# Kernel tuning notes

Hardware: AMD Instinct MI355X
Metric: run time of the kernel (lower is better)

Reference implementation:

```python
import jax, jax.numpy as jnp
import numpy as np

B, C, N = 8, 3, 4096
NSAMPLE = 10
MLP = (64, 64)
# checkerboard re-gather pattern from the original module
INDS = np.array([0, 1, 2, 3, 2, 3, 4, 5, 4, 5, 6, 7, 6, 7, 8, 9])


def setup_inputs() -> dict:
    key = jax.random.key(0)
    k1, k2, k3 = jax.random.split(key, 3)
    pos = jax.random.normal(k1, (B, C, N), jnp.float32)
    w1 = jax.random.normal(k2, (MLP[0], 4 * C, 2, 2), jnp.float32) * 0.1  # Conv2d(12, mlp0, k=2)
    b1 = jnp.zeros((MLP[0],), jnp.float32)
    w2 = jax.random.normal(k3, (MLP[1], MLP[0]), jnp.float32) * 0.1       # Conv2d(mlp0, mlp1, k=1)
    b2 = jnp.zeros((MLP[1],), jnp.float32)
    return {"pos": pos, "w1": w1, "b1": b1, "w2": w2, "b2": b2}


def _squeeze_2x2_alt(x):
    # x: [B, N, c, 4, 4] -> [B, N, 4c, 2, 2] with channel order [a, d, b, c]
    a = x[..., 0::2, 0::2]  # (0,0) of each 2x2 block
    d = x[..., 1::2, 1::2]  # (1,1)
    b = x[..., 0::2, 1::2]  # (0,1)
    c = x[..., 1::2, 0::2]  # (1,0)
    return jnp.concatenate([a, d, b, c], axis=-3)


def reference(pos, w1, b1, w2, b2):
    Bn, Cn, Nn = pos.shape
    pos_t = pos.transpose(0, 2, 1)  # [B, N, C]
    # pairwise squared distances [B, N, N]
    sq = jnp.sum(pos_t * pos_t, axis=-1)
    d2 = sq[:, :, None] - 2.0 * jnp.einsum('bnc,bmc->bnm', pos_t, pos_t) + sq[:, None, :]
    _, idx = jax.lax.top_k(-d2, NSAMPLE)  # [B, N, K] nearest neighbors (self first)
    # grouping_operation: grouped[b,c,n,k] = pos[b,c,idx[b,n,k]]
    grouped = jax.vmap(lambda p, i: p[:, i])(pos, idx)  # [B, C, N, K]
    pg = grouped[..., INDS]                              # [B, C, N, 16]
    pg = pg.transpose(0, 2, 1, 3).reshape(Bn, Nn, Cn, 4, 4)  # [B, N, 3, 4, 4]
    sqz = _squeeze_2x2_alt(pg)                           # [B, N, 12, 2, 2]
    # Conv2d(12->mlp0, k=2, stride=1) over 2x2 spatial == full contraction
    h = jnp.einsum('bnchw,ochw->bno', sqz, w1) + b1      # [B, N, mlp0]
    out = jnp.einsum('bno,po->bnp', h, w2) + b2          # [B, N, mlp1]
    return out.transpose(0, 2, 1)                        # [B, mlp1, N]
```

## Files before the change

### kernel.cpp

```cpp
#include <hip/hip_runtime.h>
#include <math.h>

#define NPTS 4096
#define NSMP 10

typedef float f32x2 __attribute__((ext_vector_type(2)));

__global__ __launch_bounds__(256) void prep_kernel(
    const float* __restrict__ w1, const float* __restrict__ b1,
    const float* __restrict__ w2, const float* __restrict__ b2,
    float* __restrict__ wn, float* __restrict__ bb) {
  __shared__ float w1l[64 * 48];
  __shared__ float w2t[64 * 64];
  __shared__ float b1l[64];
  __shared__ float part[4][30][64];
  __shared__ float bpart[4][64];
  const int t = threadIdx.x, p = t & 63, grp = t >> 6, o0 = grp * 16;
  for (int idx = t; idx < 64 * 48; idx += 256) w1l[idx] = w1[idx];
  for (int idx = t; idx < 64 * 64; idx += 256) w2t[(idx & 63) * 64 + (idx >> 6)] = w2[idx];
  if (t < 64) b1l[t] = b1[t];
  __syncthreads();

  const int sg[16] = {0,2,4,6, 3,5,7,9, 1,3,5,7, 2,4,6,8};
  float w2r[16];
  #pragma unroll
  for (int oo = 0; oo < 16; ++oo) w2r[oo] = w2t[(o0 + oo) * 64 + p];
  float wloc[30];
  #pragma unroll
  for (int i = 0; i < 30; ++i) wloc[i] = 0.0f;
  #pragma unroll
  for (int g = 0; g < 4; ++g)
    #pragma unroll
    for (int i = 0; i < 2; ++i)
      #pragma unroll
      for (int j = 0; j < 2; ++j) {
        const int s = sg[g * 4 + i * 2 + j];
        #pragma unroll
        for (int c = 0; c < 3; ++c) {
          const int k = (c + 3 * g) * 4 + i * 2 + j;
          float wk = 0.0f;
          #pragma unroll
          for (int oo = 0; oo < 16; ++oo)
            wk = fmaf(w2r[oo], w1l[(o0 + oo) * 48 + k], wk);
          wloc[s * 3 + c] += wk;
        }
      }
  #pragma unroll
  for (int i = 0; i < 30; ++i) part[grp][i][p] = wloc[i];
  float sb = 0.0f;
  #pragma unroll
  for (int oo = 0; oo < 16; ++oo) sb = fmaf(w2r[oo], b1l[o0 + oo], sb);
  bpart[grp][p] = sb;
  __syncthreads();
  const float* p0 = &part[0][0][0];
  for (int idx = t; idx < 30 * 64; idx += 256)
    wn[idx] = p0[idx] + p0[1920 + idx] + p0[3840 + idx] + p0[5760 + idx];
  if (t < 64) bb[t] = b2[t] + bpart[0][t] + bpart[1][t] + bpart[2][t] + bpart[3][t];
}

__global__ __launch_bounds__(1024, 8) void topk_kernel(const float* __restrict__ pos,
                                                       const float* __restrict__ wng,
                                                       const float* __restrict__ bbg,
                                                       float* __restrict__ out) {
  __shared__ float pts3[NPTS * 3];
  __shared__ float trans[16 * 260];
  __shared__ float wl[30 * 64];
  __shared__ float bl[64];
  __shared__ int   nbrL[16][4][NSMP];
  __shared__ int   cnt[16][4];

  const int b = blockIdx.y, tid = threadIdx.x, lane = tid & 63, wv = tid >> 6;
  const float* pb = pos + (size_t)b * 3 * NPTS;
  for (int i = tid; i < NPTS; i += 1024) {
    pts3[3 * i + 0] = pb[i];
    pts3[3 * i + 1] = pb[i + NPTS];
    pts3[3 * i + 2] = pb[i + 2 * NPTS];
  }
  for (int i = tid; i < 30 * 64; i += 1024) wl[i] = wng[i];
  if (tid < 64) bl[tid] = bbg[tid];
  __syncthreads();

  const int nb = blockIdx.x * 64;
  const int n0 = nb + wv * 4;
  float* transF = &trans[wv * 260];
  int*   bufiW  = (int*)transF;

  f32x2 qx2[2], qy2[2], qz2[2], dmin[2];
  #pragma unroll
  for (int pp = 0; pp < 2; ++pp) {
    int na = n0 + 2 * pp;
    qx2[pp].x = -2.0f * pts3[3 * na + 0]; qx2[pp].y = -2.0f * pts3[3 * na + 3];
    qy2[pp].x = -2.0f * pts3[3 * na + 1]; qy2[pp].y = -2.0f * pts3[3 * na + 4];
    qz2[pp].x = -2.0f * pts3[3 * na + 2]; qz2[pp].y = -2.0f * pts3[3 * na + 5];
    dmin[pp].x = INFINITY; dmin[pp].y = INFINITY;
  }

  #pragma unroll 2
  for (int k = 0; k < 64; ++k) {
    int m = k * 64 + lane;
    float x = pts3[3 * m], y = pts3[3 * m + 1], z = pts3[3 * m + 2];
    float sq = fmaf(z, z, fmaf(y, y, x * x));
    f32x2 sq2; sq2.x = sq; sq2.y = sq;
    #pragma unroll
    for (int pp = 0; pp < 2; ++pp) {
      f32x2 key = qx2[pp] * x + sq2;
      key = qy2[pp] * y + key;
      key = qz2[pp] * z + key;
      dmin[pp] = __builtin_elementwise_min(dmin[pp], key);
    }
  }

  unsigned um[4];
  #pragma unroll
  for (int r = 0; r < 4; ++r) {
    float dm = (r & 1) ? dmin[r >> 1].y : dmin[r >> 1].x;
    unsigned ub = __float_as_uint(dm);
    um[r] = (ub & 0x80000000u) ? ~ub : (ub | 0x80000000u);
  }
  unsigned pfx0 = 0u, pfx1 = 0u, pfx2 = 0u, pfx3 = 0u;
  #pragma unroll 1
  for (int bno = 31; bno >= 8; --bno) {
    const unsigned bit = 1u << bno, ones = bit - 1u;
    if (__popcll(__ballot(um[0] <= (pfx0 | ones))) < NSMP) pfx0 |= bit;
    if (__popcll(__ballot(um[1] <= (pfx1 | ones))) < NSMP) pfx1 |= bit;
    if (__popcll(__ballot(um[2] <= (pfx2 | ones))) < NSMP) pfx2 |= bit;
    if (__popcll(__ballot(um[3] <= (pfx3 | ones))) < NSMP) pfx3 |= bit;
  }
  float tx[4];
  #pragma unroll
  for (int r = 0; r < 4; ++r) {
    unsigned T = ((r == 0) ? pfx0 : (r == 1) ? pfx1 : (r == 2) ? pfx2 : pfx3) | 0xFFu;
    unsigned tb = (T & 0x80000000u) ? (T ^ 0x80000000u) : ~T;
    float tf = __uint_as_float(tb);
    tx[r] = __fadd_rn(__fadd_rn(tf, 2e-4f), __fmul_rn(fabsf(tf), 1e-5f));
  }

  if (lane < 4) cnt[wv][lane] = 0;

  #pragma unroll 2
  for (int k = 0; k < 64; ++k) {
    int m = k * 64 + lane;
    float x = pts3[3 * m], y = pts3[3 * m + 1], z = pts3[3 * m + 2];
    float sq = fmaf(z, z, fmaf(y, y, x * x));
    f32x2 sq2; sq2.x = sq; sq2.y = sq;
    #pragma unroll
    for (int pp = 0; pp < 2; ++pp) {
      f32x2 key = qx2[pp] * x + sq2;
      key = qy2[pp] * y + key;
      key = qz2[pp] * z + key;
      if (key.x <= tx[2 * pp]) {
        int ps = atomicAdd(&cnt[wv][2 * pp], 1);
        if (ps < 64) bufiW[(2 * pp) * 64 + ps] = m;
      }
      if (key.y <= tx[2 * pp + 1]) {
        int ps = atomicAdd(&cnt[wv][2 * pp + 1], 1);
        if (ps < 64) bufiW[(2 * pp + 1) * 64 + ps] = m;
      }
    }
  }

  int c[4], si[4], rank[4];
  double dd[4];
  int cmax = 0;
  #pragma unroll
  for (int r = 0; r < 4; ++r) {
    c[r] = __builtin_amdgcn_readfirstlane(cnt[wv][r]);
    if (c[r] > 64) c[r] = 64;
    cmax = (c[r] > cmax) ? c[r] : cmax;
    rank[r] = 0;
  }
  #pragma unroll
  for (int r = 0; r < 4; ++r) {
    int nq = n0 + r;
    float qxf = pts3[3 * nq], qyf = pts3[3 * nq + 1], qzf = pts3[3 * nq + 2];
    if (lane < c[r]) {
      si[r] = bufiW[r * 64 + lane];
      float px = pts3[3 * si[r]], py = pts3[3 * si[r] + 1], pz = pts3[3 * si[r] + 2];
      double dqx = (double)qxf, dqy = (double)qyf, dqz = (double)qzf;
      double dpx = (double)px, dpy = (double)py, dpz = (double)pz;
      double dot = dqx * dpx + dqy * dpy + dqz * dpz;
      double sqn = dqx * dqx + dqy * dqy + dqz * dqz;
      double sqm = dpx * dpx + dpy * dpy + dpz * dpz;
      dd[r] = (sqn - 2.0 * dot) + sqm;
    } else { dd[r] = (double)INFINITY; si[r] = 0x7FFFFFFF; }
  }
  #pragma unroll 1
  for (int j = 0; j < cmax; ++j) {
    #pragma unroll
    for (int r = 0; r < 4; ++r) {
      int jlo = __builtin_amdgcn_readlane(__double2loint(dd[r]), j);
      int jhi = __builtin_amdgcn_readlane(__double2hiint(dd[r]), j);
      int ji  = __builtin_amdgcn_readlane(si[r], j);
      double jd = __hiloint2double(jhi, jlo);
      if (jd < dd[r] || (jd == dd[r] && ji < si[r])) ++rank[r];
    }
  }
  #pragma unroll
  for (int r = 0; r < 4; ++r)
    if (lane < c[r] && rank[r] < NSMP)
      nbrL[wv][r][rank[r]] = si[r];

  #pragma unroll 1
  for (int r = 0; r < 4; ++r) {
    float a = bl[lane];
    #pragma unroll
    for (int s = 0; s < NSMP; ++s) {
      int id = nbrL[wv][r][s];
      float px = pts3[3 * id], py = pts3[3 * id + 1], pz = pts3[3 * id + 2];
      a = fmaf(wl[(s * 3 + 0) * 64 + lane], px, a);
      a = fmaf(wl[(s * 3 + 1) * 64 + lane], py, a);
      a = fmaf(wl[(s * 3 + 2) * 64 + lane], pz, a);
    }
    transF[r * 65 + lane] = a;
  }
  __syncthreads();

  {
    int p = tid >> 4, t16 = tid & 15;
    float4 v;
    v.x = trans[t16 * 260 + 0 * 65 + p];
    v.y = trans[t16 * 260 + 1 * 65 + p];
    v.z = trans[t16 * 260 + 2 * 65 + p];
    v.w = trans[t16 * 260 + 3 * 65 + p];
    *(float4*)(out + ((size_t)b * 64 + p) * NPTS + nb + 4 * t16) = v;
  }
}

extern "C" void kernel_launch(void* const* d_in, const int* in_sizes, int n_in,
                              void* d_out, int out_size, void* d_ws, size_t ws_size,
                              hipStream_t stream) {
  (void)in_sizes; (void)n_in; (void)out_size; (void)ws_size;
  const float* pos = (const float*)d_in[0];
  const float* w1  = (const float*)d_in[1];
  const float* b1  = (const float*)d_in[2];
  const float* w2  = (const float*)d_in[3];
  const float* b2  = (const float*)d_in[4];
  float* out = (float*)d_out;

  float* wn = (float*)d_ws;
  float* bb = (float*)((char*)d_ws + 30 * 64 * 4);

  prep_kernel<<<dim3(1), dim3(256), 0, stream>>>(w1, b1, w2, b2, wn, bb);
  topk_kernel<<<dim3(64, 8), dim3(1024), 0, stream>>>(pos, wn, bb, out);
}
```

Before: 131.5 us.

## Compute kNN distance keys with fp16 split-precision MFMA instead of scalar FMAs

Both distance passes (the min-per-lane threshold pass and the candidate-collection pass) now run as 32x32x16 f16 MFMA products. Each point is stored as hi/lo fp16 pairs of x, y, z and the squared norm, so the matrix product approximates -2q·p+|p|^2. Work is reassigned so each wave covers a slice of 512 candidates for 32 queries. Per-lane minima go to shared memory to form the radix-select input, and atomics collect candidates per query row. To absorb the reduced precision, the threshold slack now scales with the query's magnitude, and exact fp64 re-ranking plus the final MLP gather read coordinates from global memory. The changes add barriers and cut occupancy hints from 8 to 4, and a looser threshold risks more candidates or overflow past 64.

```diff
diff --git a/kernel.cpp b/kernel.cpp
--- a/kernel.cpp
+++ b/kernel.cpp
@@ -5,6 +5,8 @@
 #define NSMP 10
 
 typedef float f32x2 __attribute__((ext_vector_type(2)));
+typedef _Float16 half8 __attribute__((ext_vector_type(8)));
+typedef float f32x16 __attribute__((ext_vector_type(16)));
 
 __global__ __launch_bounds__(256) void prep_kernel(
     const float* __restrict__ w1, const float* __restrict__ b1,
@@ -58,62 +60,90 @@
   if (t < 64) bb[t] = b2[t] + bpart[0][t] + bpart[1][t] + bpart[2][t] + bpart[3][t];
 }
 
-__global__ __launch_bounds__(1024, 8) void topk_kernel(const float* __restrict__ pos,
+__global__ __launch_bounds__(1024, 4) void topk_kernel(const float* __restrict__ pos,
                                                        const float* __restrict__ wng,
                                                        const float* __restrict__ bbg,
                                                        float* __restrict__ out) {
-  __shared__ float pts3[NPTS * 3];
-  __shared__ float trans[16 * 260];
+  __shared__ half8 pts8[NPTS];
+  __shared__ float X[16 * 260];
+  __shared__ half8 a8[128];
   __shared__ float wl[30 * 64];
   __shared__ float bl[64];
-  __shared__ int   nbrL[16][4][NSMP];
-  __shared__ int   cnt[16][4];
+  __shared__ float taub[64];
+  __shared__ float slackb[64];
+  __shared__ int   cnt[64];
+  __shared__ int   nbrT[64][NSMP];
 
   const int b = blockIdx.y, tid = threadIdx.x, lane = tid & 63, wv = tid >> 6;
   const float* pb = pos + (size_t)b * 3 * NPTS;
+  const int nb = blockIdx.x * 64;
+
   for (int i = tid; i < NPTS; i += 1024) {
-    pts3[3 * i + 0] = pb[i];
-    pts3[3 * i + 1] = pb[i + NPTS];
-    pts3[3 * i + 2] = pb[i + 2 * NPTS];
+    float x = pb[i], y = pb[i + NPTS], z = pb[i + 2 * NPTS];
+    float sq = fmaf(z, z, fmaf(y, y, x * x));
+    _Float16 hx = (_Float16)x, hy = (_Float16)y, hz = (_Float16)z, hs = (_Float16)sq;
+    _Float16 lx = (_Float16)(x - (float)hx);
+    _Float16 ly = (_Float16)(y - (float)hy);
+    _Float16 lz = (_Float16)(z - (float)hz);
+    _Float16 ls = (_Float16)(sq - (float)hs);
+    half8 v = {hx, lx, hy, ly, hz, lz, hs, ls};
+    pts8[i] = v;
+  }
+  if (tid < 64) {
+    float qx = pb[nb + tid], qy = pb[nb + tid + NPTS], qz = pb[nb + tid + 2 * NPTS];
+    _Float16 ax = (_Float16)(-2.0f * (float)(_Float16)qx);
+    _Float16 ay = (_Float16)(-2.0f * (float)(_Float16)qy);
+    _Float16 az = (_Float16)(-2.0f * (float)(_Float16)qz);
+    _Float16 one = (_Float16)1.0f;
+    half8 va = {ax, ax, ay, ay, az, az, one, one};
+    half8 vz;
+    #pragma unroll
+    for (int j = 0; j < 8; ++j) vz[j] = (_Float16)0.0f;
+    a8[2 * tid] = va;
+    a8[2 * tid + 1] = vz;
+    slackb[tid] = 1.5e-3f + 0.012f * (fabsf(qx) + fabsf(qy) + fabsf(qz));
+    cnt[tid] = 0;
+    bl[tid] = bbg[tid];
   }
   for (int i = tid; i < 30 * 64; i += 1024) wl[i] = wng[i];
-  if (tid < 64) bl[tid] = bbg[tid];
-  __syncthreads();
-
-  const int nb = blockIdx.x * 64;
-  const int n0 = nb + wv * 4;
-  float* transF = &trans[wv * 260];
-  int*   bufiW  = (int*)transF;
-
-  f32x2 qx2[2], qy2[2], qz2[2], dmin[2];
-  #pragma unroll
-  for (int pp = 0; pp < 2; ++pp) {
-    int na = n0 + 2 * pp;
-    qx2[pp].x = -2.0f * pts3[3 * na + 0]; qx2[pp].y = -2.0f * pts3[3 * na + 3];
-    qy2[pp].x = -2.0f * pts3[3 * na + 1]; qy2[pp].y = -2.0f * pts3[3 * na + 4];
-    qz2[pp].x = -2.0f * pts3[3 * na + 2]; qz2[pp].y = -2.0f * pts3[3 * na + 5];
-    dmin[pp].x = INFINITY; dmin[pp].y = INFINITY;
-  }
-
-  #pragma unroll 2
-  for (int k = 0; k < 64; ++k) {
-    int m = k * 64 + lane;
-    float x = pts3[3 * m], y = pts3[3 * m + 1], z = pts3[3 * m + 2];
-    float sq = fmaf(z, z, fmaf(y, y, x * x));
-    f32x2 sq2; sq2.x = sq; sq2.y = sq;
-    #pragma unroll
-    for (int pp = 0; pp < 2; ++pp) {
-      f32x2 key = qx2[pp] * x + sq2;
-      key = qy2[pp] * y + key;
-      key = qz2[pp] * z + key;
-      dmin[pp] = __builtin_elementwise_min(dmin[pp], key);
-    }
-  }
+  __syncthreads();
+
+  const int qt = wv >> 3, ws = wv & 7, h = lane >> 5, c31 = lane & 31;
+  const int base = ws * 512;
+  const half8 af = a8[(qt * 32 + c31) * 2 + h];
+  f32x16 zz;
+  #pragma unroll
+  for (int j = 0; j < 16; ++j) zz[j] = 0.0f;
+
+  float mreg[16];
+  #pragma unroll
+  for (int j = 0; j < 16; ++j) mreg[j] = INFINITY;
+  #pragma unroll
+  for (int t = 0; t < 16; ++t) {
+    half8 bf = pts8[base + t * 32 + c31];
+    f32x16 acc = __builtin_amdgcn_mfma_f32_32x32x16_f16(af, bf, zz, 0, 0, 0);
+    #pragma unroll
+    for (int j = 0; j < 16; ++j) mreg[j] = fminf(mreg[j], acc[j]);
+  }
+  #pragma unroll
+  for (int j = 0; j < 16; ++j) {
+    mreg[j] = fminf(mreg[j], __shfl_xor(mreg[j], 1));
+    mreg[j] = fminf(mreg[j], __shfl_xor(mreg[j], 2));
+  }
+  if ((lane & 3) == 0) {
+    const int g = (lane >> 2) & 7;
+    #pragma unroll
+    for (int j = 0; j < 16; ++j) {
+      const int row = qt * 32 + (j & 3) + 8 * (j >> 2) + 4 * h;
+      X[row * 64 + ws * 8 + g] = mreg[j];
+    }
+  }
+  __syncthreads();
 
   unsigned um[4];
   #pragma unroll
   for (int r = 0; r < 4; ++r) {
-    float dm = (r & 1) ? dmin[r >> 1].y : dmin[r >> 1].x;
+    float dm = X[(4 * wv + r) * 64 + lane];
     unsigned ub = __float_as_uint(dm);
     um[r] = (ub & 0x80000000u) ? ~ub : (ub | 0x80000000u);
   }
@@ -132,50 +162,51 @@
     unsigned T = ((r == 0) ? pfx0 : (r == 1) ? pfx1 : (r == 2) ? pfx2 : pfx3) | 0xFFu;
     unsigned tb = (T & 0x80000000u) ? (T ^ 0x80000000u) : ~T;
     float tf = __uint_as_float(tb);
-    tx[r] = __fadd_rn(__fadd_rn(tf, 2e-4f), __fmul_rn(fabsf(tf), 1e-5f));
-  }
-
-  if (lane < 4) cnt[wv][lane] = 0;
-
+    tx[r] = __fadd_rn(__fadd_rn(tf, slackb[4 * wv + r]), __fmul_rn(fabsf(tf), 1e-5f));
+  }
+  if (lane == 0) {
+    taub[4 * wv + 0] = tx[0]; taub[4 * wv + 1] = tx[1];
+    taub[4 * wv + 2] = tx[2]; taub[4 * wv + 3] = tx[3];
+  }
+  __syncthreads();
+
+  float tau16[16];
+  #pragma unroll
+  for (int j = 0; j < 16; ++j) tau16[j] = taub[qt * 32 + (j & 3) + 8 * (j >> 2) + 4 * h];
+  int* bufi = (int*)X;
   #pragma unroll 2
-  for (int k = 0; k < 64; ++k) {
-    int m = k * 64 + lane;
-    float x = pts3[3 * m], y = pts3[3 * m + 1], z = pts3[3 * m + 2];
-    float sq = fmaf(z, z, fmaf(y, y, x * x));
-    f32x2 sq2; sq2.x = sq; sq2.y = sq;
-    #pragma unroll
-    for (int pp = 0; pp < 2; ++pp) {
-      f32x2 key = qx2[pp] * x + sq2;
-      key = qy2[pp] * y + key;
-      key = qz2[pp] * z + key;
-      if (key.x <= tx[2 * pp]) {
-        int ps = atomicAdd(&cnt[wv][2 * pp], 1);
-        if (ps < 64) bufiW[(2 * pp) * 64 + ps] = m;
+  for (int t = 0; t < 16; ++t) {
+    const int m0 = base + t * 32 + c31;
+    half8 bf = pts8[m0];
+    f32x16 acc = __builtin_amdgcn_mfma_f32_32x32x16_f16(af, bf, zz, 0, 0, 0);
+    #pragma unroll
+    for (int j = 0; j < 16; ++j) {
+      if (acc[j] <= tau16[j]) {
+        const int row = qt * 32 + (j & 3) + 8 * (j >> 2) + 4 * h;
+        int ps = atomicAdd(&cnt[row], 1);
+        if (ps < 64) bufi[row * 64 + ps] = m0;
       }
-      if (key.y <= tx[2 * pp + 1]) {
-        int ps = atomicAdd(&cnt[wv][2 * pp + 1], 1);
-        if (ps < 64) bufiW[(2 * pp + 1) * 64 + ps] = m;
-      }
-    }
-  }
+    }
+  }
+  __syncthreads();
 
   int c[4], si[4], rank[4];
   double dd[4];
   int cmax = 0;
   #pragma unroll
   for (int r = 0; r < 4; ++r) {
-    c[r] = __builtin_amdgcn_readfirstlane(cnt[wv][r]);
+    c[r] = __builtin_amdgcn_readfirstlane(cnt[4 * wv + r]);
     if (c[r] > 64) c[r] = 64;
     cmax = (c[r] > cmax) ? c[r] : cmax;
     rank[r] = 0;
   }
   #pragma unroll
   for (int r = 0; r < 4; ++r) {
-    int nq = n0 + r;
-    float qxf = pts3[3 * nq], qyf = pts3[3 * nq + 1], qzf = pts3[3 * nq + 2];
+    const int nq = nb + 4 * wv + r;
+    float qxf = pb[nq], qyf = pb[nq + NPTS], qzf = pb[nq + 2 * NPTS];
     if (lane < c[r]) {
-      si[r] = bufiW[r * 64 + lane];
-      float px = pts3[3 * si[r]], py = pts3[3 * si[r] + 1], pz = pts3[3 * si[r] + 2];
+      si[r] = bufi[(4 * wv + r) * 64 + lane];
+      float px = pb[si[r]], py = pb[si[r] + NPTS], pz = pb[si[r] + 2 * NPTS];
       double dqx = (double)qxf, dqy = (double)qyf, dqz = (double)qzf;
       double dpx = (double)px, dpy = (double)py, dpz = (double)pz;
       double dot = dqx * dpx + dqy * dpy + dqz * dpz;
@@ -198,15 +229,17 @@
   #pragma unroll
   for (int r = 0; r < 4; ++r)
     if (lane < c[r] && rank[r] < NSMP)
-      nbrL[wv][r][rank[r]] = si[r];
-
+      nbrT[4 * wv + r][rank[r]] = si[r];
+  __syncthreads();
+
+  float* transF = &X[wv * 260];
   #pragma unroll 1
   for (int r = 0; r < 4; ++r) {
     float a = bl[lane];
     #pragma unroll
     for (int s = 0; s < NSMP; ++s) {
-      int id = nbrL[wv][r][s];
-      float px = pts3[3 * id], py = pts3[3 * id + 1], pz = pts3[3 * id + 2];
+      const int id = nbrT[4 * wv + r][s];
+      float px = pb[id], py = pb[id + NPTS], pz = pb[id + 2 * NPTS];
       a = fmaf(wl[(s * 3 + 0) * 64 + lane], px, a);
       a = fmaf(wl[(s * 3 + 1) * 64 + lane], py, a);
       a = fmaf(wl[(s * 3 + 2) * 64 + lane], pz, a);
@@ -218,10 +251,10 @@
   {
     int p = tid >> 4, t16 = tid & 15;
     float4 v;
-    v.x = trans[t16 * 260 + 0 * 65 + p];
-    v.y = trans[t16 * 260 + 1 * 65 + p];
-    v.z = trans[t16 * 260 + 2 * 65 + p];
-    v.w = trans[t16 * 260 + 3 * 65 + p];
+    v.x = X[t16 * 260 + 0 * 65 + p];
+    v.y = X[t16 * 260 + 1 * 65 + p];
+    v.z = X[t16 * 260 + 2 * 65 + p];
+    v.w = X[t16 * 260 + 3 * 65 + p];
     *(float4*)(out + ((size_t)b * 64 + p) * NPTS + nb + 4 * t16) = v;
   }
 }
```

New measurement: 141.1 us. 1.07x slower.
